# Kernel tuning notes

Measured on AMD Instinct MI355X. Metric: run time of the kernel, lower is better.

## Reference

```python
import jax, jax.numpy as jnp
import numpy as np

NUM_HEADS = 16
HIDDEN = 1024
HEAD = HIDDEN // NUM_HEADS
NEG_INF = -10000.0


def setup_inputs() -> dict:
    key = jax.random.key(0)
    k1, k2, k3, k4 = jax.random.split(key, 4)
    B, S = 4, 2048
    x = jax.random.normal(k1, (B, S, HIDDEN), dtype=jnp.float32)
    pos_embeds = jax.random.normal(k2, (S, HIDDEN), dtype=jnp.float32)
    # Dense(3*hidden, use_bias=False) and Dense(hidden, use_bias=False)
    Wqkv = jax.random.normal(k3, (HIDDEN, 3 * HIDDEN), dtype=jnp.float32) / np.sqrt(HIDDEN)
    Wo = jax.random.normal(k4, (HIDDEN, HIDDEN), dtype=jnp.float32) / np.sqrt(HIDDEN)
    return {"x": x, "pos_embeds": pos_embeds, "Wqkv": Wqkv, "Wo": Wo}


def _compute_qkv(t, Wqkv):
    # rearrange '... s (k n h) -> k ... n s h', k=3, n=NUM_HEADS
    proj = t @ Wqkv  # [..., s, 3*n*h]
    proj = proj.reshape(*t.shape[:-1], 3, NUM_HEADS, HEAD)  # [..., s, 3, n, h]
    # move: k first, then leading dims, then n, s, h
    nd = proj.ndim
    perm = (nd - 3,) + tuple(range(nd - 4)) + (nd - 2, nd - 4, nd - 1)
    return jnp.transpose(proj, perm)  # [3, ..., n, s, h]


def reference(x, pos_embeds, Wqkv, Wo):
    S = x.shape[-2]
    q, k, v = _compute_qkv(x, Wqkv)  # each [B, n, S, h]
    pos_qkv = _compute_qkv(pos_embeds[:S], Wqkv)  # [3, n, S, h]
    pos_q, pos_k = pos_qkv[0], pos_qkv[1]
    q = q + pos_q  # broadcast over batch
    k = k + pos_k
    scores = jnp.einsum('bnqh,bnkh->bnqk', q, k) / np.sqrt(HEAD).astype(np.float32)
    causal = jnp.arange(S)[:, None] < jnp.arange(S)[None, :]  # strict upper triangle (future)
    scores = jnp.where(causal, NEG_INF, scores)
    probs = jax.nn.softmax(scores, axis=-1)
    # dropout deterministic (training=False) -> identity
    combined = jnp.einsum('bnqk,bnkh->bnqh', probs, v)  # [B, n, S, h]
    combined = jnp.transpose(combined, (0, 2, 1, 3)).reshape(x.shape[0], S, HIDDEN)  # '... n q h -> ... q (n h)'
    out = combined @ Wo
    return out
```

## Files before the change

kernel.cpp:

```cpp
#include <hip/hip_runtime.h>


typedef float f32x4 __attribute__((ext_vector_type(4)));
typedef short bf16x8 __attribute__((ext_vector_type(8)));
typedef short bf16x4 __attribute__((ext_vector_type(4)));

#define MFMA_BF16(a, b, c) __builtin_amdgcn_mfma_f32_16x16x32_bf16((a), (b), (c), 0, 0, 0)

#if __has_builtin(__builtin_amdgcn_mfma_f32_16x16x16bf16_1k)
#define HAVE_MFMA16 1
#define MFMA_BF16_K16(a, b, c) __builtin_amdgcn_mfma_f32_16x16x16bf16_1k((a), (b), (c), 0, 0, 0)
#else
#define HAVE_MFMA16 0
#endif

__device__ __forceinline__ short f2bf(float f) {
  union { float f; unsigned u; } v; v.f = f;
  unsigned u = v.u;
  u += 0x7fffu + ((u >> 16) & 1u);
  return (short)(u >> 16);
}

__device__ __forceinline__ float bf2f(short s) {
  union { unsigned u; float f; } v;
  v.u = ((unsigned)(unsigned short)s) << 16;
  return v.f;
}

__device__ __forceinline__ float fast_exp2(float x) {
#if __has_builtin(__builtin_amdgcn_exp2f)
  return __builtin_amdgcn_exp2f(x);
#else
  return exp2f(x);
#endif
}

__device__ __forceinline__ int cvt_pk_bf16(float lo, float hi) {
  int r;
  asm("v_cvt_pk_bf16_f32 %0, %1, %2" : "=v"(r) : "v"(lo), "v"(hi));
  return r;
}

__device__ __forceinline__ void gl_lds16(const short* g, short* l) {
  __builtin_amdgcn_global_load_lds(
      (const __attribute__((address_space(1))) unsigned*)(g),
      (__attribute__((address_space(3))) unsigned*)(l), 16, 0, 0);
}

__device__ __forceinline__ int swzK(int row, int colbyte) {
  return row * 64 + (((colbyte) ^ ((row & 7) << 4)) >> 1);
}
__device__ __forceinline__ int swzV(int row, int colbyte) {
  return row * 64 + ((((colbyte >> 3) + row) & 15) << 2);
}
__device__ __forceinline__ int swzE(int row, int col) {
  return row * 128 + ((((col >> 3) ^ (row & 15)) << 3) | (col & 7));
}

__device__ const int QT_X[30] = {5,6,7,8,9,10,11,11,12,12,13,13,14,14,15,15,
                                 4,10, 3,9,15, 2,8,14, 1,7,13, 0,6,12};
__device__ const int CH_X[30] = {0,0,0,0,0,0,0,1,0,1,0,1,0,1,0,1,
                                 0,1, 0,1,2, 0,1,2, 0,1,2, 0,1,2};
__device__ const int START_QT[16] = {0,1,2,3,4,5,6,8,10,12,14,16,18,21,24,27};

__global__ __launch_bounds__(256) void prep_x(const float* __restrict__ x,
                                              const float* __restrict__ pos,
                                              short* __restrict__ xb,
                                              short* __restrict__ xpb) {
  int i = blockIdx.x * 256 + threadIdx.x;
  int idx = i * 4;
  const float4 xv = *(const float4*)(x + idx);
  const float4 pv = *(const float4*)(pos + (idx & ((2048 * 1024) - 1)));
  short4 a, b;
  a.x = f2bf(xv.x); a.y = f2bf(xv.y); a.z = f2bf(xv.z); a.w = f2bf(xv.w);
  b.x = f2bf(xv.x + pv.x); b.y = f2bf(xv.y + pv.y);
  b.z = f2bf(xv.z + pv.z); b.w = f2bf(xv.w + pv.w);
  *(short4*)(xb + idx) = a;
  *(short4*)(xpb + idx) = b;
}

__global__ __launch_bounds__(256) void transpose_w2(const float* __restrict__ wqkv,
                                                    const float* __restrict__ wo,
                                                    short* __restrict__ outqkv,
                                                    short* __restrict__ outo) {
  __shared__ float tile[32][33];
  const int bx = blockIdx.x;
  const float* __restrict__ in = (bx < 96) ? wqkv : wo;
  short* __restrict__ out = (bx < 96) ? outqkv : outo;
  const int N = (bx < 96) ? 3072 : 1024;
  const int n0 = ((bx < 96) ? bx : (bx - 96)) * 32;
  const int k0 = blockIdx.y * 32;
  int c = threadIdx.x & 31, r0 = threadIdx.x >> 5;
  for (int i = 0; i < 4; i++) {
    int r = r0 + i * 8;
    tile[r][c] = in[(size_t)(k0 + r) * N + n0 + c];
  }
  __syncthreads();
  for (int i = 0; i < 4; i++) {
    int r = r0 + i * 8;
    out[(size_t)(n0 + r) * 1024 + k0 + c] = f2bf(tile[c][r]);
  }
}

__global__ __launch_bounds__(256) void gemm_qkv(const short* __restrict__ xb,
                                                const short* __restrict__ xpb,
                                                const short* __restrict__ wt,
                                                short* __restrict__ qg,
                                                short* __restrict__ kg,
                                                short* __restrict__ vtg) {
  __shared__ __align__(16) short Sh[16384];
  short* As = Sh;
  short* Bs = Sh + 8192;
  const int n = blockIdx.x;
  const int idx = n >> 3;
  const int bm = (n & 7) * 8 + (idx & 7);
  const int bn = idx >> 3;
  const short* __restrict__ A = (bn < 16) ? xpb : xb;
  const int tid = threadIdx.x;
  const int lane = tid & 63, wid = tid >> 6;
  const int wm = wid & 1, wn = wid >> 1;
  const int quad = lane >> 4, l16 = lane & 15;
  const f32x4 fzero = {0.f, 0.f, 0.f, 0.f};
  f32x4 acc[4][4];
  for (int mt = 0; mt < 4; mt++)
    for (int nt = 0; nt < 4; nt++) acc[mt][nt] = fzero;
  const int arow0 = bm * 128, brow0 = bn * 128;
  for (int k0 = 0; k0 < 1024; k0 += 64) {
#pragma unroll
    for (int i = 0; i < 4; i++) {
      int p = (wid * 4 + i) * 64 + lane;
      int row = p >> 3;
      int sch = (p & 7) ^ (row & 7);
      short* ldsb = Sh + (wid * 4 + i) * 512;
      gl_lds16(A + (size_t)(arow0 + row) * 1024 + k0 + sch * 8, ldsb);
      gl_lds16(wt + (size_t)(brow0 + row) * 1024 + k0 + sch * 8, ldsb + 8192);
    }
    __syncthreads();
    for (int ks = 0; ks < 2; ks++) {
      bf16x8 af[4], bfr[4];
      for (int mt = 0; mt < 4; mt++)
        af[mt] = *(const bf16x8*)(As + swzK(wm * 64 + mt * 16 + l16, ks * 64 + quad * 16));
      for (int nt = 0; nt < 4; nt++)
        bfr[nt] = *(const bf16x8*)(Bs + swzK(wn * 64 + nt * 16 + l16, ks * 64 + quad * 16));
      for (int mt = 0; mt < 4; mt++)
        for (int nt = 0; nt < 4; nt++)
          acc[mt][nt] = MFMA_BF16(af[mt], bfr[nt], acc[mt][nt]);
    }
    __syncthreads();
  }

  short* Sf = Sh;
  const int kk = bn >> 3;
  const int bglob = (bm * 128) >> 11;
  const int s0v = (bm * 128) & 2047;
  if (kk == 2) {
#pragma unroll
    for (int mt = 0; mt < 4; mt++)
#pragma unroll
      for (int nt = 0; nt < 4; nt++) {
        int col = wn * 64 + nt * 16 + l16;
        int sb = wm * 64 + mt * 16 + quad * 4;
        int2 pk;
        pk.x = cvt_pk_bf16(acc[mt][nt][0], acc[mt][nt][1]);
        pk.y = cvt_pk_bf16(acc[mt][nt][2], acc[mt][nt][3]);
        *(int2*)(Sf + swzE(col, sb)) = pk;
      }
    __syncthreads();
    const int col = tid >> 1, half = tid & 1;
    int head = (bn * 2 + (col >> 6)) & 15;
    int hh = col & 63;
    int4* dst = (int4*)(vtg + (size_t)((bglob * 16 + head) * 64 + hh) * 2048 + s0v + half * 64);
#pragma unroll
    for (int c = 0; c < 8; c++)
      dst[c] = *(const int4*)(Sf + swzE(col, half * 64 + c * 8));
  } else {
    const float scale = (kk == 0) ? 0.18033688f : 1.0f;
#pragma unroll
    for (int mt = 0; mt < 4; mt++)
#pragma unroll
      for (int nt = 0; nt < 4; nt++) {
        int col = wn * 64 + nt * 16 + l16;
#pragma unroll
        for (int r = 0; r < 4; r++) {
          int s_loc = wm * 64 + mt * 16 + quad * 4 + r;
          Sf[swzE(s_loc, col)] = f2bf(acc[mt][nt][r] * scale);
        }
      }
    __syncthreads();
    const int row = tid >> 1, half = tid & 1;
    int head = (bn * 2 + half) & 15;
    short* __restrict__ dstp = (kk == 0) ? qg : kg;
    int4* dst = (int4*)(dstp + (size_t)((bglob * 16 + head) * 2048 + s0v + row) * 64);
#pragma unroll
    for (int c = 0; c < 8; c++)
      dst[c] = *(const int4*)(Sf + swzE(row, half * 64 + c * 8));
  }
}

__global__ __launch_bounds__(256, 3) void attn_part(const short* __restrict__ qg,
                                                    const short* __restrict__ kg,
                                                    const short* __restrict__ vtg,
                                                    short* __restrict__ pO,
                                                    float* __restrict__ pL) {
  const int n = blockIdx.x;
  const int i = n >> 3;
  const int bh = (n & 7) * 8 + i / 30;
  const int slot = i % 30;
  const int qt = QT_X[slot], ch = CH_X[slot];
  const int p = bh * 30 + START_QT[qt] + ch;
  const short* __restrict__ Q = qg + (size_t)bh * 2048 * 64;
  const short* __restrict__ K = kg + (size_t)bh * 2048 * 64;
  const short* __restrict__ VT = vtg + (size_t)bh * 64 * 2048;
  __shared__ __align__(16) short KV[2][64 * 64];
  short* Ks = &KV[0][0];
  short* Vs = &KV[1][0];
#if !HAVE_MFMA16
  __shared__ __align__(16) short Ps[4][16 * 72];
#endif
  const int tid = threadIdx.x, lane = tid & 63, w = tid >> 6;
  const int quad = lane >> 4, l16 = lane & 15;
  const f32x4 fzero = {0.f, 0.f, 0.f, 0.f};

  bf16x8 bq[2][2];
#pragma unroll
  for (int sub = 0; sub < 2; sub++) {
    int qrow = qt * 128 + w * 32 + sub * 16 + l16;
#pragma unroll
    for (int ks = 0; ks < 2; ks++)
      bq[sub][ks] = *(const bf16x8*)(Q + (size_t)qrow * 64 + ks * 32 + quad * 8);
  }
  f32x4 acco[2][4];
  f32x4 lrun[2];
#pragma unroll
  for (int sub = 0; sub < 2; sub++) {
    for (int nt = 0; nt < 4; nt++) acco[sub][nt] = fzero;
    lrun[sub] = fzero;
  }

  const int kt0 = ch * 12;
  const int kt1 = min(kt0 + 12, 2 * qt + 2);
  const int qmin_w = qt * 128 + w * 32;

  const int sr0 = tid >> 3, sr1 = sr0 + 32;
  const int scs = (tid & 7) * 8;
  const int scb = (tid & 7) * 16;
  const int oK0 = swzK(sr0, scb), oK1 = swzK(sr1, scb);
  const int oV0a = swzV(sr0, scb), oV0b = swzV(sr0, scb + 8);
  const int oV1a = swzV(sr1, scb), oV1b = swzV(sr1, scb + 8);

  int4 kreg[2], vreg[2];
  {
    int kv0 = kt0 * 64;
    kreg[0] = *(const int4*)(K + (size_t)(kv0 + sr0) * 64 + scs);
    kreg[1] = *(const int4*)(K + (size_t)(kv0 + sr1) * 64 + scs);
    vreg[0] = *(const int4*)(VT + (size_t)sr0 * 2048 + kv0 + scs);
    vreg[1] = *(const int4*)(VT + (size_t)sr1 * 2048 + kv0 + scs);
  }

  for (int kt = kt0; kt < kt1; kt++) {
    if (kt > kt0) __syncthreads();
    *(int4*)(&Ks[oK0]) = kreg[0];
    *(int4*)(&Ks[oK1]) = kreg[1];
    *(int2*)(&Vs[oV0a]) = make_int2(vreg[0].x, vreg[0].y);
    *(int2*)(&Vs[oV0b]) = make_int2(vreg[0].z, vreg[0].w);
    *(int2*)(&Vs[oV1a]) = make_int2(vreg[1].x, vreg[1].y);
    *(int2*)(&Vs[oV1b]) = make_int2(vreg[1].z, vreg[1].w);
    __syncthreads();

    if (kt + 1 < kt1) {
      int kv0 = (kt + 1) * 64;
      kreg[0] = *(const int4*)(K + (size_t)(kv0 + sr0) * 64 + scs);
      kreg[1] = *(const int4*)(K + (size_t)(kv0 + sr1) * 64 + scs);
      vreg[0] = *(const int4*)(VT + (size_t)sr0 * 2048 + kv0 + scs);
      vreg[1] = *(const int4*)(VT + (size_t)sr1 * 2048 + kv0 + scs);
    }

    if (kt * 64 <= qmin_w + 31) {
      f32x4 accs[2][4];
#pragma unroll
      for (int sub = 0; sub < 2; sub++)
        for (int nt = 0; nt < 4; nt++) accs[sub][nt] = fzero;
      __builtin_amdgcn_s_setprio(1);
#pragma unroll
      for (int ks = 0; ks < 2; ks++)
#pragma unroll
        for (int nt = 0; nt < 4; nt++) {
          bf16x8 ak = *(const bf16x8*)(&Ks[swzK(nt * 16 + l16, ks * 64 + quad * 16)]);
          accs[0][nt] = MFMA_BF16(ak, bq[0][ks], accs[0][nt]);
          accs[1][nt] = MFMA_BF16(ak, bq[1][ks], accs[1][nt]);
        }
      __builtin_amdgcn_s_setprio(0);

      if ((kt + 1) * 64 > qmin_w) {
#pragma unroll
        for (int sub = 0; sub < 2; sub++) {
          int q = qmin_w + sub * 16 + l16;
#pragma unroll
          for (int nt = 0; nt < 4; nt++) {
            int kv = kt * 64 + nt * 16 + quad * 4;
#pragma unroll
            for (int r = 0; r < 4; r++)
              if (kv + r > q) accs[sub][nt][r] = -1e30f;
          }
        }
      }

#pragma unroll
      for (int sub = 0; sub < 2; sub++)
#pragma unroll
        for (int nt = 0; nt < 4; nt++) {
#pragma unroll
          for (int r = 0; r < 4; r++) accs[sub][nt][r] = fast_exp2(accs[sub][nt][r]);
          lrun[sub] += accs[sub][nt];
        }

#if HAVE_MFMA16
      __builtin_amdgcn_s_setprio(1);
#pragma unroll
      for (int kkk = 0; kkk < 4; kkk++) {
        union { int2 i2; bf16x4 v; } p0, p1;
        p0.i2.x = cvt_pk_bf16(accs[0][kkk][0], accs[0][kkk][1]);
        p0.i2.y = cvt_pk_bf16(accs[0][kkk][2], accs[0][kkk][3]);
        p1.i2.x = cvt_pk_bf16(accs[1][kkk][0], accs[1][kkk][1]);
        p1.i2.y = cvt_pk_bf16(accs[1][kkk][2], accs[1][kkk][3]);
#pragma unroll
        for (int nth = 0; nth < 4; nth++) {
          bf16x4 av = *(const bf16x4*)(&Vs[swzV(nth * 16 + l16, kkk * 32 + quad * 8)]);
          acco[0][nth] = MFMA_BF16_K16(av, p0.v, acco[0][nth]);
          acco[1][nth] = MFMA_BF16_K16(av, p1.v, acco[1][nth]);
        }
      }
      __builtin_amdgcn_s_setprio(0);
#else
      short* P = Ps[w];
#pragma unroll
      for (int sub = 0; sub < 2; sub++) {
#pragma unroll
        for (int nt = 0; nt < 4; nt++) {
          int2 pk;
          pk.x = cvt_pk_bf16(accs[sub][nt][0], accs[sub][nt][1]);
          pk.y = cvt_pk_bf16(accs[sub][nt][2], accs[sub][nt][3]);
          *(int2*)(P + l16 * 72 + nt * 16 + quad * 4) = pk;
        }
#pragma unroll
        for (int ks2 = 0; ks2 < 2; ks2++) {
          bf16x8 bp = *(const bf16x8*)(P + l16 * 72 + ks2 * 32 + quad * 8);
#pragma unroll
          for (int nth = 0; nth < 4; nth++) {
            int r = nth * 16 + l16;
            int4 t4;
            *(int2*)&t4.x = *(const int2*)(&Vs[swzV(r, ks2 * 64 + quad * 16)]);
            *(int2*)&t4.z = *(const int2*)(&Vs[swzV(r, ks2 * 64 + quad * 16 + 8)]);
            bf16x8 av = *(const bf16x8*)&t4;
            acco[sub][nth] = MFMA_BF16(av, bp, acco[sub][nth]);
          }
        }
      }
#endif
    }
  }

#pragma unroll
  for (int sub = 0; sub < 2; sub++) {
    float lh = (lrun[sub][0] + lrun[sub][1]) + (lrun[sub][2] + lrun[sub][3]);
    lh += __shfl_xor(lh, 16);
    lh += __shfl_xor(lh, 32);
    int qloc = w * 32 + sub * 16 + l16;
    if (quad == 0) pL[p * 128 + qloc] = lh;
  }

  __syncthreads();
  short* Ob = &KV[0][0];
#pragma unroll
  for (int sub = 0; sub < 2; sub++) {
    int qloc = w * 32 + sub * 16 + l16;
#pragma unroll
    for (int nth = 0; nth < 4; nth++) {
      int2 pk;
      pk.x = cvt_pk_bf16(acco[sub][nth][0], acco[sub][nth][1]);
      pk.y = cvt_pk_bf16(acco[sub][nth][2], acco[sub][nth][3]);
      *(int2*)(Ob + swzK(qloc, nth * 32 + quad * 8)) = pk;
    }
  }
  __syncthreads();
  {
    const int row = tid >> 1;
    const int hb = (tid & 1) * 64;
    int4 v0 = *(const int4*)(Ob + swzK(row, hb));
    int4 v1 = *(const int4*)(Ob + swzK(row, hb + 16));
    int4 v2 = *(const int4*)(Ob + swzK(row, hb + 32));
    int4 v3 = *(const int4*)(Ob + swzK(row, hb + 48));
    int4* dst = (int4*)(pO + (size_t)p * 8192 + tid * 32);
    dst[0] = v0; dst[1] = v1; dst[2] = v2; dst[3] = v3;
  }
}

__global__ __launch_bounds__(256) void attn_merge(const short* __restrict__ pO,
                                                  const float* __restrict__ pL,
                                                  short* __restrict__ comb) {
  const int n = blockIdx.x;
  const int i = n >> 3;
  const int bh = (n & 7) * 8 + (i >> 4);
  const int qt = i & 15;
  const int head = bh & 15, b = bh >> 4;
  const int nch = (2 * qt + 13) / 12;
  const int p0 = bh * 30 + START_QT[qt];
  const int t = threadIdx.x;
  const int qloc = t >> 1, hh = (t & 1) * 32;

  float l = 0.f;
  for (int c = 0; c < nch; c++) l += pL[(p0 + c) * 128 + qloc];
  const float inv = 1.f / l;

  float acc[32];
#pragma unroll
  for (int j = 0; j < 32; j++) acc[j] = 0.f;
  for (int c = 0; c < nch; c++) {
    const short* src = pO + (size_t)(p0 + c) * 8192 + (size_t)qloc * 64 + hh;
#pragma unroll
    for (int v = 0; v < 4; v++) {
      short4 d0 = *(const short4*)(src + v * 8);
      short4 d1 = *(const short4*)(src + v * 8 + 4);
      acc[v * 8 + 0] += bf2f(d0.x); acc[v * 8 + 1] += bf2f(d0.y);
      acc[v * 8 + 2] += bf2f(d0.z); acc[v * 8 + 3] += bf2f(d0.w);
      acc[v * 8 + 4] += bf2f(d1.x); acc[v * 8 + 5] += bf2f(d1.y);
      acc[v * 8 + 6] += bf2f(d1.z); acc[v * 8 + 7] += bf2f(d1.w);
    }
  }
  size_t base = (size_t)(b * 2048 + qt * 128 + qloc) * 1024 + head * 64 + hh;
#pragma unroll
  for (int v = 0; v < 8; v++) {
    short4 sv;
    sv.x = f2bf(acc[v * 4 + 0] * inv);
    sv.y = f2bf(acc[v * 4 + 1] * inv);
    sv.z = f2bf(acc[v * 4 + 2] * inv);
    sv.w = f2bf(acc[v * 4 + 3] * inv);
    *(short4*)(comb + base + v * 4) = sv;
  }
}

__global__ __launch_bounds__(256) void gemm_out(const short* __restrict__ A,
                                                const short* __restrict__ wt,
                                                float* __restrict__ out) {
  __shared__ __align__(16) short Sh[16384];
  short* As = Sh;
  short* Bs = Sh + 8192;
  const int n = blockIdx.x;
  const int idx = n >> 3;
  const int bm = (n & 7) * 8 + (idx & 7);
  const int bn = idx >> 3;
  const int tid = threadIdx.x;
  const int lane = tid & 63, wid = tid >> 6;
  const int wm = wid & 1, wn = wid >> 1;
  const int quad = lane >> 4, l16 = lane & 15;
  const f32x4 fzero = {0.f, 0.f, 0.f, 0.f};
  f32x4 acc[4][4];
  for (int mt = 0; mt < 4; mt++)
    for (int nt = 0; nt < 4; nt++) acc[mt][nt] = fzero;
  const int arow0 = bm * 128, brow0 = bn * 128;
  for (int k0 = 0; k0 < 1024; k0 += 64) {
#pragma unroll
    for (int i = 0; i < 4; i++) {
      int p = (wid * 4 + i) * 64 + lane;
      int row = p >> 3;
      int sch = (p & 7) ^ (row & 7);
      short* ldsb = Sh + (wid * 4 + i) * 512;
      gl_lds16(A + (size_t)(arow0 + row) * 1024 + k0 + sch * 8, ldsb);
      gl_lds16(wt + (size_t)(brow0 + row) * 1024 + k0 + sch * 8, ldsb + 8192);
    }
    __syncthreads();
    for (int ks = 0; ks < 2; ks++) {
      bf16x8 af[4], bfr[4];
      for (int mt = 0; mt < 4; mt++)
        af[mt] = *(const bf16x8*)(As + swzK(wm * 64 + mt * 16 + l16, ks * 64 + quad * 16));
      for (int nt = 0; nt < 4; nt++)
        bfr[nt] = *(const bf16x8*)(Bs + swzK(wn * 64 + nt * 16 + l16, ks * 64 + quad * 16));
      for (int mt = 0; mt < 4; mt++)
        for (int nt = 0; nt < 4; nt++)
          acc[mt][nt] = MFMA_BF16(af[mt], bfr[nt], acc[mt][nt]);
    }
    __syncthreads();
  }
  for (int nt = 0; nt < 4; nt++) {
    int col = bn * 128 + wn * 64 + nt * 16 + l16;
    for (int mt = 0; mt < 4; mt++) {
      int rowb = bm * 128 + wm * 64 + mt * 16 + quad * 4;
      for (int r = 0; r < 4; r++)
        out[(size_t)(rowb + r) * 1024 + col] = acc[mt][nt][r];
    }
  }
}

extern "C" void kernel_launch(void* const* d_in, const int* in_sizes, int n_in,
                              void* d_out, int out_size, void* d_ws, size_t ws_size,
                              hipStream_t stream) {
  const float* x    = (const float*)d_in[0];
  const float* pos  = (const float*)d_in[1];
  const float* Wqkv = (const float*)d_in[2];
  const float* Wo   = (const float*)d_in[3];
  float* out = (float*)d_out;

  char* ws = (char*)d_ws;
  const size_t SZ = (size_t)8192 * 1024 * 2;
  short* xb    = (short*)(ws);
  short* xpb   = (short*)(ws + SZ);
  short* pO    = (short*)(ws);
  float* pL    = (float*)(ws + (size_t)1920 * 8192 * 2);
  short* q     = (short*)(ws + 2 * SZ);
  short* k     = (short*)(ws + 3 * SZ);
  short* vt    = (short*)(ws + 4 * SZ);
  short* comb  = (short*)(ws + 5 * SZ);
  short* wqkvt = (short*)(ws + 6 * SZ);
  short* wot   = (short*)(ws + 6 * SZ + (size_t)3072 * 1024 * 2);

  prep_x<<<8192, 256, 0, stream>>>(x, pos, xb, xpb);
  transpose_w2<<<dim3(128, 32), 256, 0, stream>>>(Wqkv, Wo, wqkvt, wot);
  gemm_qkv<<<dim3(1536), 256, 0, stream>>>(xb, xpb, wqkvt, q, k, vt);
  attn_part<<<dim3(1920), 256, 0, stream>>>(q, k, vt, pO, pL);
  attn_merge<<<dim3(1024), 256, 0, stream>>>(pO, pL, comb);
  gemm_out<<<dim3(512), 256, 0, stream>>>(comb, wot, out);
}
```

Measured before the change: 287.3 us.

## Double-buffer LDS tiles in QKV and output GEMMs with K=32 stages

Both GEMM kernels now split the K loop into 32-wide steps and alternate between two LDS buffers within the same shared allocation. The next tile is prefetched with global_load_lds while MFMAs run on the current one, so global latency overlaps compute. A new 4-row XOR swizzle fits the narrower tiles. The cost is half as much MFMA work per barrier and twice as many synchronisations.

```diff
diff --git a/kernel.cpp b/kernel.cpp
--- a/kernel.cpp
+++ b/kernel.cpp
@@ -49,6 +49,9 @@
 
 __device__ __forceinline__ int swzK(int row, int colbyte) {
   return row * 64 + (((colbyte) ^ ((row & 7) << 4)) >> 1);
+}
+__device__ __forceinline__ int swz32(int row, int colbyte) {
+  return row * 32 + (((colbyte) ^ ((row & 3) << 4)) >> 1);
 }
 __device__ __forceinline__ int swzV(int row, int colbyte) {
   return row * 64 + ((((colbyte >> 3) + row) & 15) << 2);
@@ -109,8 +112,6 @@
                                                 short* __restrict__ kg,
                                                 short* __restrict__ vtg) {
   __shared__ __align__(16) short Sh[16384];
-  short* As = Sh;
-  short* Bs = Sh + 8192;
   const int n = blockIdx.x;
   const int idx = n >> 3;
   const int bm = (n & 7) * 8 + (idx & 7);
@@ -125,27 +126,53 @@
   for (int mt = 0; mt < 4; mt++)
     for (int nt = 0; nt < 4; nt++) acc[mt][nt] = fzero;
   const int arow0 = bm * 128, brow0 = bn * 128;
-  for (int k0 = 0; k0 < 1024; k0 += 64) {
-#pragma unroll
-    for (int i = 0; i < 4; i++) {
-      int p = (wid * 4 + i) * 64 + lane;
-      int row = p >> 3;
-      int sch = (p & 7) ^ (row & 7);
-      short* ldsb = Sh + (wid * 4 + i) * 512;
-      gl_lds16(A + (size_t)(arow0 + row) * 1024 + k0 + sch * 8, ldsb);
-      gl_lds16(wt + (size_t)(brow0 + row) * 1024 + k0 + sch * 8, ldsb + 8192);
-    }
-    __syncthreads();
-    for (int ks = 0; ks < 2; ks++) {
-      bf16x8 af[4], bfr[4];
-      for (int mt = 0; mt < 4; mt++)
-        af[mt] = *(const bf16x8*)(As + swzK(wm * 64 + mt * 16 + l16, ks * 64 + quad * 16));
-      for (int nt = 0; nt < 4; nt++)
-        bfr[nt] = *(const bf16x8*)(Bs + swzK(wn * 64 + nt * 16 + l16, ks * 64 + quad * 16));
-      for (int mt = 0; mt < 4; mt++)
-        for (int nt = 0; nt < 4; nt++)
-          acc[mt][nt] = MFMA_BF16(af[mt], bfr[nt], acc[mt][nt]);
-    }
+
+  int prow[2], pcol[2], pbase[2];
+#pragma unroll
+  for (int i = 0; i < 2; i++) {
+    int p = (wid * 2 + i) * 64 + lane;
+    prow[i] = p >> 2;
+    pcol[i] = ((p & 3) ^ ((p >> 2) & 3)) * 8;
+    pbase[i] = (wid * 2 + i) * 512;
+  }
+
+#define STAGE_QKV(BUF, K0)                                                    \
+  {                                                                           \
+    _Pragma("unroll")                                                         \
+    for (int i = 0; i < 2; i++) {                                             \
+      gl_lds16(A + (size_t)(arow0 + prow[i]) * 1024 + (K0) + pcol[i],         \
+               Sh + (BUF)*8192 + pbase[i]);                                   \
+      gl_lds16(wt + (size_t)(brow0 + prow[i]) * 1024 + (K0) + pcol[i],        \
+               Sh + (BUF)*8192 + 4096 + pbase[i]);                            \
+    }                                                                         \
+  }
+
+#define COMPUTE_QKV(BASE)                                                     \
+  {                                                                           \
+    const short* As_ = (BASE);                                                \
+    const short* Bs_ = (BASE) + 4096;                                         \
+    bf16x8 af[4], bfr[4];                                                     \
+    _Pragma("unroll")                                                         \
+    for (int mt = 0; mt < 4; mt++)                                            \
+      af[mt] = *(const bf16x8*)(As_ + swz32(wm * 64 + mt * 16 + l16, quad * 16)); \
+    _Pragma("unroll")                                                         \
+    for (int nt = 0; nt < 4; nt++)                                            \
+      bfr[nt] = *(const bf16x8*)(Bs_ + swz32(wn * 64 + nt * 16 + l16, quad * 16)); \
+    _Pragma("unroll")                                                         \
+    for (int mt = 0; mt < 4; mt++)                                            \
+      _Pragma("unroll")                                                       \
+      for (int nt = 0; nt < 4; nt++)                                          \
+        acc[mt][nt] = MFMA_BF16(af[mt], bfr[nt], acc[mt][nt]);                \
+  }
+
+  STAGE_QKV(0, 0);
+  __syncthreads();
+  for (int t = 0; t < 32; t += 2) {
+    if (t + 1 < 32) STAGE_QKV(1, (t + 1) * 32);
+    COMPUTE_QKV(Sh);
+    __syncthreads();
+    if (t + 2 < 32) STAGE_QKV(0, (t + 2) * 32);
+    COMPUTE_QKV(Sh + 8192);
     __syncthreads();
   }
 
@@ -443,8 +470,6 @@
                                                 const short* __restrict__ wt,
                                                 float* __restrict__ out) {
   __shared__ __align__(16) short Sh[16384];
-  short* As = Sh;
-  short* Bs = Sh + 8192;
   const int n = blockIdx.x;
   const int idx = n >> 3;
   const int bm = (n & 7) * 8 + (idx & 7);
@@ -458,29 +483,56 @@
   for (int mt = 0; mt < 4; mt++)
     for (int nt = 0; nt < 4; nt++) acc[mt][nt] = fzero;
   const int arow0 = bm * 128, brow0 = bn * 128;
-  for (int k0 = 0; k0 < 1024; k0 += 64) {
-#pragma unroll
-    for (int i = 0; i < 4; i++) {
-      int p = (wid * 4 + i) * 64 + lane;
-      int row = p >> 3;
-      int sch = (p & 7) ^ (row & 7);
-      short* ldsb = Sh + (wid * 4 + i) * 512;
-      gl_lds16(A + (size_t)(arow0 + row) * 1024 + k0 + sch * 8, ldsb);
-      gl_lds16(wt + (size_t)(brow0 + row) * 1024 + k0 + sch * 8, ldsb + 8192);
-    }
-    __syncthreads();
-    for (int ks = 0; ks < 2; ks++) {
-      bf16x8 af[4], bfr[4];
-      for (int mt = 0; mt < 4; mt++)
-        af[mt] = *(const bf16x8*)(As + swzK(wm * 64 + mt * 16 + l16, ks * 64 + quad * 16));
-      for (int nt = 0; nt < 4; nt++)
-        bfr[nt] = *(const bf16x8*)(Bs + swzK(wn * 64 + nt * 16 + l16, ks * 64 + quad * 16));
-      for (int mt = 0; mt < 4; mt++)
-        for (int nt = 0; nt < 4; nt++)
-          acc[mt][nt] = MFMA_BF16(af[mt], bfr[nt], acc[mt][nt]);
-    }
-    __syncthreads();
-  }
+
+  int prow[2], pcol[2], pbase[2];
+#pragma unroll
+  for (int i = 0; i < 2; i++) {
+    int p = (wid * 2 + i) * 64 + lane;
+    prow[i] = p >> 2;
+    pcol[i] = ((p & 3) ^ ((p >> 2) & 3)) * 8;
+    pbase[i] = (wid * 2 + i) * 512;
+  }
+
+#define STAGE_OUT(BUF, K0)                                                    \
+  {                                                                           \
+    _Pragma("unroll")                                                         \
+    for (int i = 0; i < 2; i++) {                                             \
+      gl_lds16(A + (size_t)(arow0 + prow[i]) * 1024 + (K0) + pcol[i],         \
+               Sh + (BUF)*8192 + pbase[i]);                                   \
+      gl_lds16(wt + (size_t)(brow0 + prow[i]) * 1024 + (K0) + pcol[i],        \
+               Sh + (BUF)*8192 + 4096 + pbase[i]);                            \
+    }                                                                         \
+  }
+
+#define COMPUTE_OUT(BASE)                                                     \
+  {                                                                           \
+    const short* As_ = (BASE);                                                \
+    const short* Bs_ = (BASE) + 4096;                                         \
+    bf16x8 af[4], bfr[4];                                                     \
+    _Pragma("unroll")                                                         \
+    for (int mt = 0; mt < 4; mt++)                                            \
+      af[mt] = *(const bf16x8*)(As_ + swz32(wm * 64 + mt * 16 + l16, quad * 16)); \
+    _Pragma("unroll")                                                         \
+    for (int nt = 0; nt < 4; nt++)                                            \
+      bfr[nt] = *(const bf16x8*)(Bs_ + swz32(wn * 64 + nt * 16 + l16, quad * 16)); \
+    _Pragma("unroll")                                                         \
+    for (int mt = 0; mt < 4; mt++)                                            \
+      _Pragma("unroll")                                                       \
+      for (int nt = 0; nt < 4; nt++)                                          \
+        acc[mt][nt] = MFMA_BF16(af[mt], bfr[nt], acc[mt][nt]);                \
+  }
+
+  STAGE_OUT(0, 0);
+  __syncthreads();
+  for (int t = 0; t < 32; t += 2) {
+    if (t + 1 < 32) STAGE_OUT(1, (t + 1) * 32);
+    COMPUTE_OUT(Sh);
+    __syncthreads();
+    if (t + 2 < 32) STAGE_OUT(0, (t + 2) * 32);
+    COMPUTE_OUT(Sh + 8192);
+    __syncthreads();
+  }
+
   for (int nt = 0; nt < 4; nt++) {
     int col = bn * 128 + wn * 64 + nt * 16 + l16;
     for (int mt = 0; mt < 4; mt++) {
```

Result: faster. 277.8 us (-3.3%).
